# Performance work log

Measured on AMD Instinct MI355X. Metric: run time of the kernel, lower is better.

Reference implementation:

```python
import jax, jax.numpy as jnp
import numpy as np
import math

HIDDEN = 1024
HEADS = 16
HEAD_DIM = HIDDEN // HEADS
B, S = 4, 2048


def setup_inputs() -> dict:
    key = jax.random.key(0)
    ks = jax.random.split(key, 9)
    std = 1.0 / math.sqrt(HIDDEN)
    return {
        "query": jax.random.normal(ks[0], (B, S, HIDDEN), jnp.float32),
        "key": jax.random.normal(ks[1], (B, S, HIDDEN), jnp.float32),
        "value": jax.random.normal(ks[2], (B, S, HIDDEN), jnp.float32),
        "q_w": jax.random.normal(ks[3], (HIDDEN, HIDDEN), jnp.float32) * std,
        "q_b": jax.random.normal(ks[4], (HIDDEN,), jnp.float32) * 0.02,
        "k_w": jax.random.normal(ks[5], (HIDDEN, HIDDEN), jnp.float32) * std,
        "k_b": jax.random.normal(ks[6], (HIDDEN,), jnp.float32) * 0.02,
        "v_w": jax.random.normal(ks[7], (HIDDEN, HIDDEN), jnp.float32) * std,
        "v_b": jax.random.normal(ks[8], (HIDDEN,), jnp.float32) * 0.02,
    }


def _split_heads(x):
    # [B, S, H] -> [B, heads, S, head_dim]
    b, s, _ = x.shape
    return x.reshape(b, s, HEADS, HEAD_DIM).transpose(0, 2, 1, 3)


def reference(query, key, value, q_w, q_b, k_w, k_b, v_w, v_b):
    # Linear projections (torch Linear: x @ W^T + b; here weights stored as [in, out])
    q = _split_heads(query @ q_w + q_b)   # [B, h, S, d]
    k = _split_heads(key @ k_w + k_b)
    v = _split_heads(value @ v_w + v_b)
    scale = 1.0 / math.sqrt(HEAD_DIM)
    scores = jnp.einsum("bhqd,bhkd->bhqk", q, k) * scale  # [B, h, S, S]
    # NOTE: faithful to source bug — context uses raw scaled scores, NOT softmax probs.
    # (softmax is computed in the original but its result is unused for the output.)
    ctx = jnp.einsum("bhqk,bhkd->bhqd", scores, v)
    ctx = ctx.transpose(0, 2, 1, 3).reshape(query.shape[0], query.shape[1], HIDDEN)
    return ctx
```

## Files before the change

### kernel.cpp

```cpp
#include <hip/hip_runtime.h>
#include <stdint.h>

#define HIDDEN 1024
#define HEADS 16
#define HEAD_DIM 64
#define BATCH 4
#define SEQ 2048
#define ROWS (BATCH * SEQ)

typedef float f32x4 __attribute__((ext_vector_type(4)));
typedef short bf16x8 __attribute__((ext_vector_type(8)));

__device__ __forceinline__ uint16_t f32_to_bf16_rne(float f) {
    uint32_t u = __float_as_uint(f);
    uint32_t r = u + 0x7FFFu + ((u >> 16) & 1u);
    return (uint16_t)(r >> 16);
}
__device__ __forceinline__ float bf16_to_f32(uint16_t u) {
    return __uint_as_float(((uint32_t)u) << 16);
}

__global__ __launch_bounds__(256) void cvt_kernel(const float* __restrict__ Xq,
                                                  const float* __restrict__ Xk,
                                                  const float* __restrict__ Xv,
                                                  uint16_t* __restrict__ Xb) {
    int z = blockIdx.x >> 12;
    const float* X = z == 0 ? Xq : (z == 1 ? Xk : Xv);
    uint16_t* out = Xb + (size_t)z * ROWS * HIDDEN;
    size_t e = ((size_t)(blockIdx.x & 4095) * 256 + threadIdx.x) * 8;
    float4 f0 = *(const float4*)(X + e);
    float4 f1 = *(const float4*)(X + e + 4);
    uint4 pk;
    pk.x = (uint32_t)f32_to_bf16_rne(f0.x) | ((uint32_t)f32_to_bf16_rne(f0.y) << 16);
    pk.y = (uint32_t)f32_to_bf16_rne(f0.z) | ((uint32_t)f32_to_bf16_rne(f0.w) << 16);
    pk.z = (uint32_t)f32_to_bf16_rne(f1.x) | ((uint32_t)f32_to_bf16_rne(f1.y) << 16);
    pk.w = (uint32_t)f32_to_bf16_rne(f1.z) | ((uint32_t)f32_to_bf16_rne(f1.w) << 16);
    *(uint4*)(out + e) = pk;
}

__global__ __launch_bounds__(256) void wt_kernel(const float* __restrict__ Wk,
                                                 const float* __restrict__ Wv,
                                                 uint16_t* __restrict__ Wt) {
    const float* W = blockIdx.z == 0 ? Wk : Wv;
    uint16_t* out = Wt + (size_t)blockIdx.z * HIDDEN * HIDDEN;
    __shared__ float tile[64][65];
    int k0 = blockIdx.x * 64, n0 = blockIdx.y * 64;
    int r = threadIdx.x >> 6, c = threadIdx.x & 63;
    for (int it = 0; it < 16; ++it) {
        int rr = r + 4 * it;
        tile[rr][c] = W[(size_t)(k0 + rr) * HIDDEN + n0 + c];
    }
    __syncthreads();
    for (int it = 0; it < 16; ++it) {
        int rr = r + 4 * it;
        out[(size_t)(n0 + rr) * HIDDEN + k0 + c] = f32_to_bf16_rne(tile[c][rr]);
    }
}


#define STAGE(GSRC, CHUNKBASE)                                                   \
    {                                                                            \
        _Pragma("unroll") for (int l = 0; l < 2; ++l) {                          \
            int gb = l * 512 + w * 64;              \
            int g = gb + lane;                                                   \
            int r = g >> 3;                                                      \
            int c = (g & 7) ^ (r & 7);                                           \
            __builtin_amdgcn_global_load_lds(                                    \
                (const __attribute__((address_space(1))) uint32_t*)((GSRC) +     \
                    (size_t)r * HIDDEN + c * 8),                                 \
                (__attribute__((address_space(3))) uint32_t*)(&lds[((CHUNKBASE) + gb) * 8]), \
                16, 0, 0);                                                       \
        }                                                                        \
    }

#define LDA(BUFU16, MH, AQ)                                                      \
    {                                                                            \
        _Pragma("unroll") for (int i = 0; i < 4; ++i) {                          \
            int ar = wm + (MH) * 64 + i * 16 + m_lane;                           \
            _Pragma("unroll") for (int ks = 0; ks < 2; ++ks) {                   \
                int p = (ks * 4 + kq) ^ (ar & 7);                                \
                AQ[i][ks] = *(const bf16x8*)(&lds[(BUFU16) + ar * 64 + p * 8]);  \
            }                                                                    \
        }                                                                        \
    }

#define LDB(BUFU16, NH, BQ)                                                      \
    {                                                                            \
        _Pragma("unroll") for (int j = 0; j < 2; ++j) {                          \
            int br = wn + (NH) * 32 + j * 16 + m_lane;                           \
            _Pragma("unroll") for (int ks = 0; ks < 2; ++ks) {                   \
                int p = (ks * 4 + kq) ^ (br & 7);                                \
                BQ[j][ks] = *(const bf16x8*)(&lds[(BUFU16) + 16384 + br * 64 + p * 8]); \
            }                                                                    \
        }                                                                        \
    }

#define MFMA_QUAD(AQ, BQ, MH, NH)                                                \
    {                                                                            \
        _Pragma("unroll") for (int ks = 0; ks < 2; ++ks)                         \
        _Pragma("unroll") for (int i = 0; i < 4; ++i)                            \
        _Pragma("unroll") for (int j = 0; j < 2; ++j)                            \
            acc[(MH) * 4 + i][(NH) * 2 + j] =                                    \
                __builtin_amdgcn_mfma_f32_16x16x32_bf16(                         \
                    AQ[i][ks], BQ[j][ks], acc[(MH) * 4 + i][(NH) * 2 + j], 0, 0, 0); \
    }

#define PHASE_MID()                                                              \
    __builtin_amdgcn_s_barrier();                                                \
    asm volatile("s_waitcnt lgkmcnt(0)" ::: "memory");                           \
    __builtin_amdgcn_s_setprio(1);

#define PHASE_END()                                                              \
    __builtin_amdgcn_s_setprio(0);                                               \
    __builtin_amdgcn_s_barrier();

__global__ __launch_bounds__(512, 1) void proj_gemm8(const uint16_t* __restrict__ Xkv,
                                                     const uint16_t* __restrict__ Wt,
                                                     const float* __restrict__ Bk,
                                                     const float* __restrict__ Bv,
                                                     uint16_t* __restrict__ KV) {
    extern __shared__ uint16_t lds[];

    const int z = blockIdx.z;
    const uint16_t* X = Xkv + (size_t)z * ROWS * HIDDEN;
    const uint16_t* W = Wt + (size_t)z * HIDDEN * HIDDEN;
    const float* bias = z == 0 ? Bk : Bv;
    uint16_t* out = KV + (size_t)z * ROWS * HIDDEN;

    const int tid = threadIdx.x;
    const int lane = tid & 63;
    const int w = tid >> 6;
    const int wm = (w >> 2) * 128;
    const int wn = (w & 3) * 64;
    const int m_lane = lane & 15;
    const int kq = lane >> 4;
    const int m0 = blockIdx.x * 256;
    const int n0 = blockIdx.y * 256;

    const uint16_t* Xb = X + (size_t)m0 * HIDDEN;
    const uint16_t* Wb = W + (size_t)n0 * HIDDEN;

    f32x4 acc[8][4] = {};
    bf16x8 aq[4][2], b0q[2][2], b1q[2][2];

    STAGE(Xb, 0);
    STAGE(Xb + 128 * HIDDEN, 1024);
    STAGE(Wb, 2048);
    STAGE(Wb + 128 * HIDDEN, 3072);
    STAGE(Wb + 64, 4096 + 2048);
    STAGE(Wb + 128 * HIDDEN + 64, 4096 + 3072);
    asm volatile("s_waitcnt vmcnt(4)" ::: "memory");
    __builtin_amdgcn_s_barrier();

#pragma unroll 1
    for (int i = 0; i < 7; ++i) {
        const int kb = i * 128;
        LDA(0, 0, aq); LDB(0, 0, b0q);
        STAGE(Xb + kb + 64, 4096 + 0);
        PHASE_MID(); MFMA_QUAD(aq, b0q, 0, 0); PHASE_END();
        LDB(0, 1, b1q);
        STAGE(Xb + 128 * HIDDEN + kb + 64, 4096 + 1024);
        PHASE_MID(); MFMA_QUAD(aq, b1q, 0, 1); PHASE_END();
        LDA(0, 1, aq);
        STAGE(Wb + kb + 128, 2048);
        PHASE_MID(); MFMA_QUAD(aq, b1q, 1, 1); PHASE_END();
        STAGE(Wb + 128 * HIDDEN + kb + 128, 3072);
        asm volatile("s_waitcnt vmcnt(4)" ::: "memory");
        __builtin_amdgcn_s_barrier();
        __builtin_amdgcn_s_setprio(1);
        MFMA_QUAD(aq, b0q, 1, 0);
        PHASE_END();
        LDA(32768, 0, aq); LDB(32768, 0, b0q);
        STAGE(Xb + kb + 128, 0);
        PHASE_MID(); MFMA_QUAD(aq, b0q, 0, 0); PHASE_END();
        LDB(32768, 1, b1q);
        STAGE(Xb + 128 * HIDDEN + kb + 128, 1024);
        PHASE_MID(); MFMA_QUAD(aq, b1q, 0, 1); PHASE_END();
        LDA(32768, 1, aq);
        STAGE(Wb + kb + 192, 4096 + 2048);
        PHASE_MID(); MFMA_QUAD(aq, b1q, 1, 1); PHASE_END();
        STAGE(Wb + 128 * HIDDEN + kb + 192, 4096 + 3072);
        asm volatile("s_waitcnt vmcnt(4)" ::: "memory");
        __builtin_amdgcn_s_barrier();
        __builtin_amdgcn_s_setprio(1);
        MFMA_QUAD(aq, b0q, 1, 0);
        PHASE_END();
    }

    {
        const int kb = 896;
        LDA(0, 0, aq); LDB(0, 0, b0q);
        STAGE(Xb + kb + 64, 4096 + 0);
        PHASE_MID(); MFMA_QUAD(aq, b0q, 0, 0); PHASE_END();
        LDB(0, 1, b1q);
        STAGE(Xb + 128 * HIDDEN + kb + 64, 4096 + 1024);
        PHASE_MID(); MFMA_QUAD(aq, b1q, 0, 1); PHASE_END();
        LDA(0, 1, aq);
        PHASE_MID(); MFMA_QUAD(aq, b1q, 1, 1); PHASE_END();
        asm volatile("s_waitcnt vmcnt(0)" ::: "memory");
        __builtin_amdgcn_s_barrier();
        __builtin_amdgcn_s_setprio(1);
        MFMA_QUAD(aq, b0q, 1, 0);
        PHASE_END();
        LDA(32768, 0, aq); LDB(32768, 0, b0q);
        PHASE_MID(); MFMA_QUAD(aq, b0q, 0, 0); PHASE_END();
        LDB(32768, 1, b1q);
        PHASE_MID(); MFMA_QUAD(aq, b1q, 0, 1); PHASE_END();
        LDA(32768, 1, aq);
        PHASE_MID(); MFMA_QUAD(aq, b1q, 1, 1); PHASE_END();
        __builtin_amdgcn_s_setprio(1);
        MFMA_QUAD(aq, b0q, 1, 0);
        __builtin_amdgcn_s_setprio(0);
    }

    for (int nj = 0; nj < 4; ++nj) {
        int col = n0 + wn + nj * 16 + m_lane;
        float bj = bias[col];
        for (int mi = 0; mi < 8; ++mi) {
            int rbase = m0 + wm + mi * 16 + kq * 4;
            for (int rg = 0; rg < 4; ++rg) {
                float v = acc[mi][nj][rg] + bj;
                out[(size_t)(rbase + rg) * HIDDEN + col] = f32_to_bf16_rne(v);
            }
        }
    }
}

__global__ __launch_bounds__(256) void kv_kernel(const uint16_t* __restrict__ KV,
                                                 float* __restrict__ P) {
    const uint16_t* K = KV;
    const uint16_t* V = KV + (size_t)ROWS * HIDDEN;
    const int bh = blockIdx.x;
    const int sc = blockIdx.y;
    const int b = bh >> 4, h = bh & 15;
    const int tid = threadIdx.x;
    const size_t base = ((size_t)b * SEQ + sc * 256) * HIDDEN + h * 64;

    __shared__ float kk[16][64];
    __shared__ float vv[16][64];
    float acc[4][4] = {};
    const int i0 = (tid >> 4) * 4, j0 = (tid & 15) * 4;

    for (int batch = 0; batch < 16; ++batch) {
        __syncthreads();
        {
            int t = tid & 127;
            int row = t >> 3, c = t & 7;
            const uint16_t* src =
                (tid < 128 ? K : V) + base + (size_t)(batch * 16 + row) * HIDDEN + c * 8;
            float* dst = (tid < 128 ? &kk[row][c * 8] : &vv[row][c * 8]);
            bf16x8 d = *(const bf16x8*)src;
            for (int e = 0; e < 8; ++e) dst[e] = bf16_to_f32((uint16_t)d[e]);
        }
        __syncthreads();
        for (int r = 0; r < 16; ++r) {
            f32x4 ka = *(const f32x4*)(&kk[r][i0]);
            f32x4 va = *(const f32x4*)(&vv[r][j0]);
            for (int a = 0; a < 4; ++a)
                for (int bb = 0; bb < 4; ++bb)
                    acc[a][bb] += ka[a] * va[bb];
        }
    }
    float* Pp = P + ((size_t)bh * 8 + sc) * 4096;
    for (int a = 0; a < 4; ++a) {
        f32x4 row;
        for (int bb = 0; bb < 4; ++bb) row[bb] = acc[a][bb] * 0.125f;
        *(f32x4*)(&Pp[(i0 + a) * 64 + j0]) = row;
    }
}

__global__ __launch_bounds__(256) void wprime_kernel(const float* __restrict__ Wq,
                                                     const float* __restrict__ bq,
                                                     const float* __restrict__ P,
                                                     uint16_t* __restrict__ Wpt,
                                                     float* __restrict__ bp) {
    const int h = blockIdx.x;
    const int r0 = blockIdx.y * 64;
    const int b = blockIdx.z;
    const int tid = threadIdx.x;

    __shared__ float Mh[64][65];
    __shared__ float Wl[64][65];
    const float* Pp = P + ((size_t)(b * 16 + h)) * 8 * 4096;
    for (int it = 0; it < 16; ++it) {
        int e = it * 256 + tid;
        int a = e >> 6, c = e & 63;
        float s = 0.f;
        for (int sc = 0; sc < 8; ++sc) s += Pp[sc * 4096 + e];
        Mh[a][c] = s;
        Wl[a][c] = Wq[(size_t)(r0 + a) * HIDDEN + h * 64 + c];
    }
    __syncthreads();

    const int r = tid & 63;
    const int jbase = tid >> 6;
    float acc[16] = {};
    for (int i = 0; i < 64; ++i) {
        float wv = Wl[r][i];
        for (int jj = 0; jj < 16; ++jj)
            acc[jj] += wv * Mh[i][jbase + 4 * jj];
    }
    uint16_t* Wb = Wpt + (size_t)b * HIDDEN * HIDDEN;
    for (int jj = 0; jj < 16; ++jj) {
        int n = h * 64 + jbase + 4 * jj;
        Wb[(size_t)n * HIDDEN + r0 + r] = f32_to_bf16_rne(acc[jj]);
    }

    if (blockIdx.y == 0 && tid < 64) {
        int j = tid;
        float s = 0.f;
        for (int i = 0; i < 64; ++i) s += bq[h * 64 + i] * Mh[i][j];
        bp[b * HIDDEN + h * 64 + j] = s;
    }
}

__global__ __launch_bounds__(256) void final_gemm(const uint16_t* __restrict__ Xq,
                                                  const uint16_t* __restrict__ Wpt,
                                                  const float* __restrict__ bp,
                                                  float* __restrict__ out) {
    __shared__ uint16_t slds[16384];

    const int tid = threadIdx.x;
    const int lane = tid & 63;
    const int w = tid >> 6;
    const int wm = (w >> 1) * 64;
    const int wn = (w & 1) * 64;
    const int m_lane = lane & 15;
    const int kq = lane >> 4;
    const int m0 = blockIdx.x * 128;
    const int n0 = blockIdx.y * 128;
    const int batch = m0 >> 11;
    const uint16_t* W = Wpt + (size_t)batch * HIDDEN * HIDDEN;
    const float* bias = bp + batch * HIDDEN;

    f32x4 acc[4][4] = {};

    for (int kb = 0; kb < HIDDEN; kb += 64) {
        for (int t = 0; t < 4; ++t) {
            int gbase = (w * 4 + t) * 64;
            int g = gbase + lane;
            int r = g >> 3;
            int c = (g & 7) ^ (r & 7);
            const uint16_t* srcA = Xq + (size_t)(m0 + r) * HIDDEN + kb + c * 8;
            __builtin_amdgcn_global_load_lds(
                (const __attribute__((address_space(1))) uint32_t*)srcA,
                (__attribute__((address_space(3))) uint32_t*)(&slds[gbase * 8]),
                16, 0, 0);
            const uint16_t* srcB = W + (size_t)(n0 + r) * HIDDEN + kb + c * 8;
            __builtin_amdgcn_global_load_lds(
                (const __attribute__((address_space(1))) uint32_t*)srcB,
                (__attribute__((address_space(3))) uint32_t*)(&slds[8192 + gbase * 8]),
                16, 0, 0);
        }
        __syncthreads();
        for (int ks = 0; ks < 2; ++ks) {
            int cbase = ks * 4 + kq;
            bf16x8 af[4], bfr[4];
            for (int i = 0; i < 4; ++i) {
                int r = wm + i * 16 + m_lane;
                int p = cbase ^ (r & 7);
                af[i] = *(const bf16x8*)(&slds[r * 64 + p * 8]);
            }
            for (int j = 0; j < 4; ++j) {
                int nr = wn + j * 16 + m_lane;
                int p = cbase ^ (nr & 7);
                bfr[j] = *(const bf16x8*)(&slds[8192 + nr * 64 + p * 8]);
            }
            for (int i = 0; i < 4; ++i)
                for (int j = 0; j < 4; ++j)
                    acc[i][j] = __builtin_amdgcn_mfma_f32_16x16x32_bf16(
                        af[i], bfr[j], acc[i][j], 0, 0, 0);
        }
        __syncthreads();
    }

    for (int j = 0; j < 4; ++j) {
        int col = n0 + wn + j * 16 + m_lane;
        float bj = bias[col];
        for (int i = 0; i < 4; ++i) {
            int rbase = m0 + wm + i * 16 + kq * 4;
            for (int rg = 0; rg < 4; ++rg)
                out[(size_t)(rbase + rg) * HIDDEN + col] = acc[i][j][rg] + bj;
        }
    }
}

extern "C" void kernel_launch(void* const* d_in, const int* in_sizes, int n_in,
                              void* d_out, int out_size, void* d_ws, size_t ws_size,
                              hipStream_t stream) {
    const float* Xq = (const float*)d_in[0];
    const float* Xk = (const float*)d_in[1];
    const float* Xv = (const float*)d_in[2];
    const float* Wq = (const float*)d_in[3];
    const float* Bq = (const float*)d_in[4];
    const float* Wk = (const float*)d_in[5];
    const float* Bk = (const float*)d_in[6];
    const float* Wv = (const float*)d_in[7];
    const float* Bv = (const float*)d_in[8];
    float* out = (float*)d_out;

    char* ws = (char*)d_ws;
    uint16_t* Xb = (uint16_t*)ws;
    uint16_t* KV = (uint16_t*)(ws + 50331648);
    uint16_t* Wt = (uint16_t*)(ws + 83886080);
    float* P = (float*)(ws + 88080384);
    uint16_t* Wpt = (uint16_t*)(ws + 96468992);
    float* bp = (float*)(ws + 104857600);

    static bool attr_done = false;
    if (!attr_done) {
        (void)hipFuncSetAttribute((const void*)proj_gemm8,
                                  hipFuncAttributeMaxDynamicSharedMemorySize, 131072);
        attr_done = true;
    }

    cvt_kernel<<<dim3(3 * 4096), 256, 0, stream>>>(Xq, Xk, Xv, Xb);
    wt_kernel<<<dim3(16, 16, 2), 256, 0, stream>>>(Wk, Wv, Wt);

    const uint16_t* Xkv = Xb + (size_t)ROWS * HIDDEN;
    proj_gemm8<<<dim3(32, 4, 2), 512, 131072, stream>>>(Xkv, Wt, Bk, Bv, KV);
    kv_kernel<<<dim3(64, 8), 256, 0, stream>>>(KV, P);
    wprime_kernel<<<dim3(16, 16, 4), 256, 0, stream>>>(Wq, Bq, P, Wpt, bp);
    final_gemm<<<dim3(64, 8), 256, 0, stream>>>(Xb, Wpt, bp, out);
}
```

Before: 276.3 us.

## Split K/V projection into separate launches and precompute LDS/global offsets

The K and V projections were one z-indexed launch of the pipelined 256x256 kernel. Now the K projection runs alone on that kernel, and the V projection runs on a simpler 128x128 single-buffered kernel. The big kernel's staging and LDS fragment loads now use per-thread precomputed pointer offsets instead of recomputing swizzled addresses each time, which cuts integer work in the inner loop. The split launch leaves only 128 blocks for K (likely under one wave per CU) and moves V to a less optimised kernel, so total projection time may rise.

```diff
diff --git a/kernel.cpp b/kernel.cpp
--- a/kernel.cpp
+++ b/kernel.cpp
@@ -60,38 +60,29 @@
 
 #define STAGE(GSRC, CHUNKBASE)                                                   \
     {                                                                            \
-        _Pragma("unroll") for (int l = 0; l < 2; ++l) {                          \
-            int gb = l * 512 + w * 64;              \
-            int g = gb + lane;                                                   \
-            int r = g >> 3;                                                      \
-            int c = (g & 7) ^ (r & 7);                                           \
-            __builtin_amdgcn_global_load_lds(                                    \
-                (const __attribute__((address_space(1))) uint32_t*)((GSRC) +     \
-                    (size_t)r * HIDDEN + c * 8),                                 \
-                (__attribute__((address_space(3))) uint32_t*)(&lds[((CHUNKBASE) + gb) * 8]), \
-                16, 0, 0);                                                       \
-        }                                                                        \
-    }
-
-#define LDA(BUFU16, MH, AQ)                                                      \
+        __builtin_amdgcn_global_load_lds(                                        \
+            (const __attribute__((address_space(1))) uint32_t*)((GSRC) + soff0), \
+            (__attribute__((address_space(3))) uint32_t*)(lds + (CHUNKBASE) * 8 + ldst0), \
+            16, 0, 0);                                                           \
+        __builtin_amdgcn_global_load_lds(                                        \
+            (const __attribute__((address_space(1))) uint32_t*)((GSRC) + soff1), \
+            (__attribute__((address_space(3))) uint32_t*)(lds + (CHUNKBASE) * 8 + ldst1), \
+            16, 0, 0);                                                           \
+    }
+
+#define LDA(BUF, MH, AQ)                                                         \
     {                                                                            \
         _Pragma("unroll") for (int i = 0; i < 4; ++i) {                          \
-            int ar = wm + (MH) * 64 + i * 16 + m_lane;                           \
-            _Pragma("unroll") for (int ks = 0; ks < 2; ++ks) {                   \
-                int p = (ks * 4 + kq) ^ (ar & 7);                                \
-                AQ[i][ks] = *(const bf16x8*)(&lds[(BUFU16) + ar * 64 + p * 8]);  \
-            }                                                                    \
+            AQ[i][0] = *(const bf16x8*)(pkA0 + (BUF) + ((MH)*64 + i*16) * 64);   \
+            AQ[i][1] = *(const bf16x8*)(pkA1 + (BUF) + ((MH)*64 + i*16) * 64);   \
         }                                                                        \
     }
 
-#define LDB(BUFU16, NH, BQ)                                                      \
+#define LDB(BUF, NH, BQ)                                                         \
     {                                                                            \
         _Pragma("unroll") for (int j = 0; j < 2; ++j) {                          \
-            int br = wn + (NH) * 32 + j * 16 + m_lane;                           \
-            _Pragma("unroll") for (int ks = 0; ks < 2; ++ks) {                   \
-                int p = (ks * 4 + kq) ^ (br & 7);                                \
-                BQ[j][ks] = *(const bf16x8*)(&lds[(BUFU16) + 16384 + br * 64 + p * 8]); \
-            }                                                                    \
+            BQ[j][0] = *(const bf16x8*)(pkB0 + (BUF) + ((NH)*32 + j*16) * 64);   \
+            BQ[j][1] = *(const bf16x8*)(pkB1 + (BUF) + ((NH)*32 + j*16) * 64);   \
         }                                                                        \
     }
 
@@ -114,18 +105,11 @@
     __builtin_amdgcn_s_setprio(0);                                               \
     __builtin_amdgcn_s_barrier();
 
-__global__ __launch_bounds__(512, 1) void proj_gemm8(const uint16_t* __restrict__ Xkv,
-                                                     const uint16_t* __restrict__ Wt,
-                                                     const float* __restrict__ Bk,
-                                                     const float* __restrict__ Bv,
-                                                     uint16_t* __restrict__ KV) {
+__global__ __launch_bounds__(512, 1) void proj_gemm8(const uint16_t* __restrict__ X,
+                                                     const uint16_t* __restrict__ W,
+                                                     const float* __restrict__ bias,
+                                                     uint16_t* __restrict__ out) {
     extern __shared__ uint16_t lds[];
-
-    const int z = blockIdx.z;
-    const uint16_t* X = Xkv + (size_t)z * ROWS * HIDDEN;
-    const uint16_t* W = Wt + (size_t)z * HIDDEN * HIDDEN;
-    const float* bias = z == 0 ? Bk : Bv;
-    uint16_t* out = KV + (size_t)z * ROWS * HIDDEN;
 
     const int tid = threadIdx.x;
     const int lane = tid & 63;
@@ -139,6 +123,22 @@
 
     const uint16_t* Xb = X + (size_t)m0 * HIDDEN;
     const uint16_t* Wb = W + (size_t)n0 * HIDDEN;
+
+    const int gA = w * 64 + lane;
+    const int rA = gA >> 3, cA = (gA & 7) ^ (rA & 7);
+    const int soff0 = rA * HIDDEN + cA * 8;
+    const int gB = 512 + w * 64 + lane;
+    const int rB = gB >> 3, cB = (gB & 7) ^ (rB & 7);
+    const int soff1 = rB * HIDDEN + cB * 8;
+    const int ldst0 = (w * 64) * 8;
+    const int ldst1 = (512 + w * 64) * 8;
+
+    const int pswz0 = (kq ^ (m_lane & 7)) * 8;
+    const int pswz1 = ((4 ^ kq) ^ (m_lane & 7)) * 8;
+    const uint16_t* pkA0 = lds + wm * 64 + m_lane * 64 + pswz0;
+    const uint16_t* pkA1 = lds + wm * 64 + m_lane * 64 + pswz1;
+    const uint16_t* pkB0 = lds + 16384 + wn * 64 + m_lane * 64 + pswz0;
+    const uint16_t* pkB1 = lds + 16384 + wn * 64 + m_lane * 64 + pswz1;
 
     f32x4 acc[8][4] = {};
     bf16x8 aq[4][2], b0q[2][2], b1q[2][2];
@@ -226,98 +226,17 @@
     }
 }
 
-__global__ __launch_bounds__(256) void kv_kernel(const uint16_t* __restrict__ KV,
-                                                 float* __restrict__ P) {
-    const uint16_t* K = KV;
-    const uint16_t* V = KV + (size_t)ROWS * HIDDEN;
-    const int bh = blockIdx.x;
-    const int sc = blockIdx.y;
-    const int b = bh >> 4, h = bh & 15;
-    const int tid = threadIdx.x;
-    const size_t base = ((size_t)b * SEQ + sc * 256) * HIDDEN + h * 64;
-
-    __shared__ float kk[16][64];
-    __shared__ float vv[16][64];
-    float acc[4][4] = {};
-    const int i0 = (tid >> 4) * 4, j0 = (tid & 15) * 4;
-
-    for (int batch = 0; batch < 16; ++batch) {
-        __syncthreads();
-        {
-            int t = tid & 127;
-            int row = t >> 3, c = t & 7;
-            const uint16_t* src =
-                (tid < 128 ? K : V) + base + (size_t)(batch * 16 + row) * HIDDEN + c * 8;
-            float* dst = (tid < 128 ? &kk[row][c * 8] : &vv[row][c * 8]);
-            bf16x8 d = *(const bf16x8*)src;
-            for (int e = 0; e < 8; ++e) dst[e] = bf16_to_f32((uint16_t)d[e]);
-        }
-        __syncthreads();
-        for (int r = 0; r < 16; ++r) {
-            f32x4 ka = *(const f32x4*)(&kk[r][i0]);
-            f32x4 va = *(const f32x4*)(&vv[r][j0]);
-            for (int a = 0; a < 4; ++a)
-                for (int bb = 0; bb < 4; ++bb)
-                    acc[a][bb] += ka[a] * va[bb];
-        }
-    }
-    float* Pp = P + ((size_t)bh * 8 + sc) * 4096;
-    for (int a = 0; a < 4; ++a) {
-        f32x4 row;
-        for (int bb = 0; bb < 4; ++bb) row[bb] = acc[a][bb] * 0.125f;
-        *(f32x4*)(&Pp[(i0 + a) * 64 + j0]) = row;
-    }
-}
-
-__global__ __launch_bounds__(256) void wprime_kernel(const float* __restrict__ Wq,
-                                                     const float* __restrict__ bq,
-                                                     const float* __restrict__ P,
-                                                     uint16_t* __restrict__ Wpt,
-                                                     float* __restrict__ bp) {
-    const int h = blockIdx.x;
-    const int r0 = blockIdx.y * 64;
-    const int b = blockIdx.z;
-    const int tid = threadIdx.x;
-
-    __shared__ float Mh[64][65];
-    __shared__ float Wl[64][65];
-    const float* Pp = P + ((size_t)(b * 16 + h)) * 8 * 4096;
-    for (int it = 0; it < 16; ++it) {
-        int e = it * 256 + tid;
-        int a = e >> 6, c = e & 63;
-        float s = 0.f;
-        for (int sc = 0; sc < 8; ++sc) s += Pp[sc * 4096 + e];
-        Mh[a][c] = s;
-        Wl[a][c] = Wq[(size_t)(r0 + a) * HIDDEN + h * 64 + c];
-    }
-    __syncthreads();
-
-    const int r = tid & 63;
-    const int jbase = tid >> 6;
-    float acc[16] = {};
-    for (int i = 0; i < 64; ++i) {
-        float wv = Wl[r][i];
-        for (int jj = 0; jj < 16; ++jj)
-            acc[jj] += wv * Mh[i][jbase + 4 * jj];
-    }
-    uint16_t* Wb = Wpt + (size_t)b * HIDDEN * HIDDEN;
-    for (int jj = 0; jj < 16; ++jj) {
-        int n = h * 64 + jbase + 4 * jj;
-        Wb[(size_t)n * HIDDEN + r0 + r] = f32_to_bf16_rne(acc[jj]);
-    }
-
-    if (blockIdx.y == 0 && tid < 64) {
-        int j = tid;
-        float s = 0.f;
-        for (int i = 0; i < 64; ++i) s += bq[h * 64 + i] * Mh[i][j];
-        bp[b * HIDDEN + h * 64 + j] = s;
-    }
-}
-
-__global__ __launch_bounds__(256) void final_gemm(const uint16_t* __restrict__ Xq,
-                                                  const uint16_t* __restrict__ Wpt,
-                                                  const float* __restrict__ bp,
-                                                  float* __restrict__ out) {
+__global__ __launch_bounds__(256) void proj_gemm(const uint16_t* __restrict__ Xkv,
+                                                 const uint16_t* __restrict__ Wt,
+                                                 const float* __restrict__ Bk,
+                                                 const float* __restrict__ Bv,
+                                                 uint16_t* __restrict__ KV) {
+    const int z = blockIdx.z;
+    const uint16_t* X = Xkv + (size_t)z * ROWS * HIDDEN;
+    const uint16_t* W = Wt + (size_t)z * HIDDEN * HIDDEN;
+    const float* bias = z == 0 ? Bk : Bv;
+    uint16_t* out = KV + (size_t)z * ROWS * HIDDEN;
+
     __shared__ uint16_t slds[16384];
 
     const int tid = threadIdx.x;
@@ -329,9 +248,6 @@
     const int kq = lane >> 4;
     const int m0 = blockIdx.x * 128;
     const int n0 = blockIdx.y * 128;
-    const int batch = m0 >> 11;
-    const uint16_t* W = Wpt + (size_t)batch * HIDDEN * HIDDEN;
-    const float* bias = bp + batch * HIDDEN;
 
     f32x4 acc[4][4] = {};
 
@@ -341,7 +257,7 @@
             int g = gbase + lane;
             int r = g >> 3;
             int c = (g & 7) ^ (r & 7);
-            const uint16_t* srcA = Xq + (size_t)(m0 + r) * HIDDEN + kb + c * 8;
+            const uint16_t* srcA = X + (size_t)(m0 + r) * HIDDEN + kb + c * 8;
             __builtin_amdgcn_global_load_lds(
                 (const __attribute__((address_space(1))) uint32_t*)srcA,
                 (__attribute__((address_space(3))) uint32_t*)(&slds[gbase * 8]),
@@ -379,6 +295,167 @@
         float bj = bias[col];
         for (int i = 0; i < 4; ++i) {
             int rbase = m0 + wm + i * 16 + kq * 4;
+            for (int rg = 0; rg < 4; ++rg) {
+                float v = acc[i][j][rg] + bj;
+                out[(size_t)(rbase + rg) * HIDDEN + col] = f32_to_bf16_rne(v);
+            }
+        }
+    }
+}
+
+__global__ __launch_bounds__(256) void kv_kernel(const uint16_t* __restrict__ KV,
+                                                 float* __restrict__ P) {
+    const uint16_t* K = KV;
+    const uint16_t* V = KV + (size_t)ROWS * HIDDEN;
+    const int bh = blockIdx.x;
+    const int sc = blockIdx.y;
+    const int b = bh >> 4, h = bh & 15;
+    const int tid = threadIdx.x;
+    const size_t base = ((size_t)b * SEQ + sc * 256) * HIDDEN + h * 64;
+
+    __shared__ float kk[16][64];
+    __shared__ float vv[16][64];
+    float acc[4][4] = {};
+    const int i0 = (tid >> 4) * 4, j0 = (tid & 15) * 4;
+
+    for (int batch = 0; batch < 16; ++batch) {
+        __syncthreads();
+        {
+            int t = tid & 127;
+            int row = t >> 3, c = t & 7;
+            const uint16_t* src =
+                (tid < 128 ? K : V) + base + (size_t)(batch * 16 + row) * HIDDEN + c * 8;
+            float* dst = (tid < 128 ? &kk[row][c * 8] : &vv[row][c * 8]);
+            bf16x8 d = *(const bf16x8*)src;
+            for (int e = 0; e < 8; ++e) dst[e] = bf16_to_f32((uint16_t)d[e]);
+        }
+        __syncthreads();
+        for (int r = 0; r < 16; ++r) {
+            f32x4 ka = *(const f32x4*)(&kk[r][i0]);
+            f32x4 va = *(const f32x4*)(&vv[r][j0]);
+            for (int a = 0; a < 4; ++a)
+                for (int bb = 0; bb < 4; ++bb)
+                    acc[a][bb] += ka[a] * va[bb];
+        }
+    }
+    float* Pp = P + ((size_t)bh * 8 + sc) * 4096;
+    for (int a = 0; a < 4; ++a) {
+        f32x4 row;
+        for (int bb = 0; bb < 4; ++bb) row[bb] = acc[a][bb] * 0.125f;
+        *(f32x4*)(&Pp[(i0 + a) * 64 + j0]) = row;
+    }
+}
+
+__global__ __launch_bounds__(256) void wprime_kernel(const float* __restrict__ Wq,
+                                                     const float* __restrict__ bq,
+                                                     const float* __restrict__ P,
+                                                     uint16_t* __restrict__ Wpt,
+                                                     float* __restrict__ bp) {
+    const int h = blockIdx.x;
+    const int r0 = blockIdx.y * 64;
+    const int b = blockIdx.z;
+    const int tid = threadIdx.x;
+
+    __shared__ float Mh[64][65];
+    __shared__ float Wl[64][65];
+    const float* Pp = P + ((size_t)(b * 16 + h)) * 8 * 4096;
+    for (int it = 0; it < 16; ++it) {
+        int e = it * 256 + tid;
+        int a = e >> 6, c = e & 63;
+        float s = 0.f;
+        for (int sc = 0; sc < 8; ++sc) s += Pp[sc * 4096 + e];
+        Mh[a][c] = s;
+        Wl[a][c] = Wq[(size_t)(r0 + a) * HIDDEN + h * 64 + c];
+    }
+    __syncthreads();
+
+    const int r = tid & 63;
+    const int jbase = tid >> 6;
+    float acc[16] = {};
+    for (int i = 0; i < 64; ++i) {
+        float wv = Wl[r][i];
+        for (int jj = 0; jj < 16; ++jj)
+            acc[jj] += wv * Mh[i][jbase + 4 * jj];
+    }
+    uint16_t* Wb = Wpt + (size_t)b * HIDDEN * HIDDEN;
+    for (int jj = 0; jj < 16; ++jj) {
+        int n = h * 64 + jbase + 4 * jj;
+        Wb[(size_t)n * HIDDEN + r0 + r] = f32_to_bf16_rne(acc[jj]);
+    }
+
+    if (blockIdx.y == 0 && tid < 64) {
+        int j = tid;
+        float s = 0.f;
+        for (int i = 0; i < 64; ++i) s += bq[h * 64 + i] * Mh[i][j];
+        bp[b * HIDDEN + h * 64 + j] = s;
+    }
+}
+
+__global__ __launch_bounds__(256) void final_gemm(const uint16_t* __restrict__ Xq,
+                                                  const uint16_t* __restrict__ Wpt,
+                                                  const float* __restrict__ bp,
+                                                  float* __restrict__ out) {
+    __shared__ uint16_t slds[16384];
+
+    const int tid = threadIdx.x;
+    const int lane = tid & 63;
+    const int w = tid >> 6;
+    const int wm = (w >> 1) * 64;
+    const int wn = (w & 1) * 64;
+    const int m_lane = lane & 15;
+    const int kq = lane >> 4;
+    const int m0 = blockIdx.x * 128;
+    const int n0 = blockIdx.y * 128;
+    const int batch = m0 >> 11;
+    const uint16_t* W = Wpt + (size_t)batch * HIDDEN * HIDDEN;
+    const float* bias = bp + batch * HIDDEN;
+
+    f32x4 acc[4][4] = {};
+
+    for (int kb = 0; kb < HIDDEN; kb += 64) {
+        for (int t = 0; t < 4; ++t) {
+            int gbase = (w * 4 + t) * 64;
+            int g = gbase + lane;
+            int r = g >> 3;
+            int c = (g & 7) ^ (r & 7);
+            const uint16_t* srcA = Xq + (size_t)(m0 + r) * HIDDEN + kb + c * 8;
+            __builtin_amdgcn_global_load_lds(
+                (const __attribute__((address_space(1))) uint32_t*)srcA,
+                (__attribute__((address_space(3))) uint32_t*)(&slds[gbase * 8]),
+                16, 0, 0);
+            const uint16_t* srcB = W + (size_t)(n0 + r) * HIDDEN + kb + c * 8;
+            __builtin_amdgcn_global_load_lds(
+                (const __attribute__((address_space(1))) uint32_t*)srcB,
+                (__attribute__((address_space(3))) uint32_t*)(&slds[8192 + gbase * 8]),
+                16, 0, 0);
+        }
+        __syncthreads();
+        for (int ks = 0; ks < 2; ++ks) {
+            int cbase = ks * 4 + kq;
+            bf16x8 af[4], bfr[4];
+            for (int i = 0; i < 4; ++i) {
+                int r = wm + i * 16 + m_lane;
+                int p = cbase ^ (r & 7);
+                af[i] = *(const bf16x8*)(&slds[r * 64 + p * 8]);
+            }
+            for (int j = 0; j < 4; ++j) {
+                int nr = wn + j * 16 + m_lane;
+                int p = cbase ^ (nr & 7);
+                bfr[j] = *(const bf16x8*)(&slds[8192 + nr * 64 + p * 8]);
+            }
+            for (int i = 0; i < 4; ++i)
+                for (int j = 0; j < 4; ++j)
+                    acc[i][j] = __builtin_amdgcn_mfma_f32_16x16x32_bf16(
+                        af[i], bfr[j], acc[i][j], 0, 0, 0);
+        }
+        __syncthreads();
+    }
+
+    for (int j = 0; j < 4; ++j) {
+        int col = n0 + wn + j * 16 + m_lane;
+        float bj = bias[col];
+        for (int i = 0; i < 4; ++i) {
+            int rbase = m0 + wm + i * 16 + kq * 4;
             for (int rg = 0; rg < 4; ++rg)
                 out[(size_t)(rbase + rg) * HIDDEN + col] = acc[i][j][rg] + bj;
         }
@@ -418,7 +495,11 @@
     wt_kernel<<<dim3(16, 16, 2), 256, 0, stream>>>(Wk, Wv, Wt);
 
     const uint16_t* Xkv = Xb + (size_t)ROWS * HIDDEN;
-    proj_gemm8<<<dim3(32, 4, 2), 512, 131072, stream>>>(Xkv, Wt, Bk, Bv, KV);
+    proj_gemm8<<<dim3(32, 4), 512, 131072, stream>>>(Xkv, Wt, Bk, KV);
+    proj_gemm<<<dim3(64, 8, 1), 256, 0, stream>>>(
+        Xkv + (size_t)ROWS * HIDDEN, Wt + (size_t)HIDDEN * HIDDEN, Bv, Bv,
+        KV + (size_t)ROWS * HIDDEN);
+
     kv_kernel<<<dim3(64, 8), 256, 0, stream>>>(KV, P);
     wprime_kernel<<<dim3(16, 16, 4), 256, 0, stream>>>(Wq, Bq, P, Wpt, bp);
     final_gemm<<<dim3(64, 8), 256, 0, stream>>>(Xb, Wpt, bp, out);
```

After: 284.8 us. 3.1% more time.
